# Kernel optimization log

Hardware: AMD Instinct MI355X
Metric: run time of the kernel (lower is better)

## Reference

```python
import jax, jax.numpy as jnp
import numpy as np
import math

H = 12   # num_attention_heads
DH = 64  # attention_head_size
HID = H * DH  # 768


def setup_inputs() -> dict:
    key = jax.random.key(0)
    ks = jax.random.split(key, 16)
    B, S = 2, 128
    inp = {
        'hidden_states': jax.random.normal(ks[0], (B, S, HID), jnp.float32),
        'attention_mask': jnp.zeros((B, 1, 1, S), jnp.float32),
        'inference_path': jax.random.normal(ks[1], (B, S, S, HID), jnp.float32),
        'span_mask': jax.random.uniform(ks[2], (B, 1, S, S), jnp.float32),
    }
    sc = 1.0 / math.sqrt(HID)
    # weights stored as [in, out]; y = x @ W + b
    inp['Wq'] = jax.random.normal(ks[3], (HID, HID), jnp.float32) * sc
    inp['bq'] = jnp.zeros((HID,), jnp.float32)
    inp['Wk'] = jax.random.normal(ks[4], (HID, HID), jnp.float32) * sc
    inp['bk'] = jnp.zeros((HID,), jnp.float32)
    inp['Wv'] = jax.random.normal(ks[5], (HID, HID), jnp.float32) * sc
    inp['bv'] = jnp.zeros((HID,), jnp.float32)
    inp['Wpv'] = jax.random.normal(ks[6], (HID, DH), jnp.float32) * sc
    inp['bpv'] = jnp.zeros((DH,), jnp.float32)
    inp['Wip'] = jax.random.normal(ks[7], (HID, 2 * HID), jnp.float32) * sc
    inp['Wmlp'] = jax.random.normal(ks[8], (HID + DH, HID), jnp.float32) * sc
    inp['bmlp'] = jnp.zeros((HID,), jnp.float32)
    return inp


def reference(hidden_states, attention_mask, inference_path, span_mask,
              Wq, bq, Wk, bk, Wv, bv, Wpv, bpv, Wip, Wmlp, bmlp):
    B, S, _ = hidden_states.shape
    # projections
    q = (hidden_states @ Wq + bq).reshape(B, S, H, DH).transpose(0, 2, 1, 3)  # [B,H,S,Dh]
    k = (hidden_states @ Wk + bk).reshape(B, S, H, DH).transpose(0, 2, 1, 3)
    v = (hidden_states @ Wv + bv).reshape(B, S, H, DH).transpose(0, 2, 1, 3)
    # parse value path: [B,1,S,Dh]
    pv = (hidden_states @ Wpv + bpv).reshape(B, S, 1, DH).transpose(0, 2, 1, 3)
    parse_ctx = jnp.matmul(span_mask, pv)              # [B,1,S,Dh]
    parse_ctx = parse_ctx.transpose(0, 2, 1, 3)        # [B,S,1,Dh]
    # relative inference-path bias: raw view (matches torch .view semantics)
    ip = inference_path @ Wip                           # [B,S,S,2*HID]
    ra, rb = jnp.split(ip, 2, axis=-1)                  # each [B,S,S,HID]
    ra = ra.reshape(B, H, S, S, DH)
    rb = rb.reshape(B, H, S, S, DH)
    qe = q[:, :, :, None, :] + ra                       # [B,H,S,S,Dh]
    ke = k[:, :, None, :, :] + rb                       # [B,H,S,S,Dh]
    scores = jnp.einsum('bhqkd,bhqkd->bhqk', qe, ke)
    scores = scores / math.sqrt(DH) + attention_mask
    probs = jax.nn.softmax(scores, axis=-1)             # dropout is identity in eval
    ctx = jnp.matmul(probs, v)                          # [B,H,S,Dh]
    ctx = ctx.transpose(0, 2, 1, 3)                     # [B,S,H,Dh]
    ctx = jnp.concatenate([ctx, parse_ctx], axis=-2)    # [B,S,H+1,Dh]
    ctx = ctx.reshape(B, S, HID + DH)
    return ctx @ Wmlp + bmlp                            # [B,S,HID]
```

## Files before the change

kernel.cpp:

```cpp
#include <hip/hip_runtime.h>
#include <hip/hip_bf16.h>


typedef __attribute__((ext_vector_type(8))) __bf16 bf16x8;
typedef __attribute__((ext_vector_type(16))) float f32x16;
typedef __attribute__((ext_vector_type(4))) float f32x4;

#define QKV_OFF   0u
#define ARENA_OFF 2424832u
#define SC_OFF    4784128u
#define CTX_OFF   6356992u

__global__ __launch_bounds__(256)
void prep_kernel(const float* __restrict__ Wip, __bf16* __restrict__ arena) {
  const int l = threadIdx.x & 63;
  const int f = blockIdx.x * 4 + (threadIdx.x >> 6);
  const int n32 = f / 48, k16 = f - n32 * 48;
  const float* src = Wip + (size_t)(k16 * 16 + (l >> 5) * 8) * 1536 + n32 * 32 + (l & 31);
  union { __bf16 h[8]; uint4 u; } pk;
#pragma unroll
  for (int j = 0; j < 8; j++) pk.h[j] = (__bf16)src[(size_t)j * 1536];
  ((uint4*)arena)[(size_t)f * 64 + l] = pk.u;
}

__global__ __launch_bounds__(64)
void proj_kernel(const float* __restrict__ hs,
                 const float* __restrict__ Wq, const float* __restrict__ bq,
                 const float* __restrict__ Wk, const float* __restrict__ bk,
                 const float* __restrict__ Wv, const float* __restrict__ bv,
                 const float* __restrict__ Wpv, const float* __restrict__ bpv,
                 float* __restrict__ qkv) {
  const int n0 = blockIdx.x * 32;
  const int m0 = blockIdx.y * 32;
  const float* W; const float* bias; int noff, ldw;
  if (n0 < 768)       { W = Wq;  bias = bq;  noff = n0;        ldw = 768; }
  else if (n0 < 1536) { W = Wk;  bias = bk;  noff = n0 - 768;  ldw = 768; }
  else if (n0 < 2304) { W = Wv;  bias = bv;  noff = n0 - 1536; ldw = 768; }
  else                { W = Wpv; bias = bpv; noff = n0 - 2304; ldw = 64;  }
  const int l = threadIdx.x;
  const int rsel = l & 31, ksel = l >> 5;
  f32x16 acc;
#pragma unroll
  for (int z = 0; z < 16; z++) acc[z] = 0.f;

#pragma unroll 4
  for (int k16 = 0; k16 < 48; k16++) {
    const float* ap = hs + (size_t)(m0 + rsel) * 768 + k16 * 16 + ksel * 8;
    float4 a0 = *(const float4*)ap;
    float4 a1 = *(const float4*)(ap + 4);
    union { __bf16 h[8]; bf16x8 v; } pa;
    pa.h[0] = (__bf16)a0.x; pa.h[1] = (__bf16)a0.y; pa.h[2] = (__bf16)a0.z; pa.h[3] = (__bf16)a0.w;
    pa.h[4] = (__bf16)a1.x; pa.h[5] = (__bf16)a1.y; pa.h[6] = (__bf16)a1.z; pa.h[7] = (__bf16)a1.w;
    const float* bp = W + (size_t)(k16 * 16 + ksel * 8) * ldw + noff + rsel;
    union { __bf16 h[8]; bf16x8 v; } pb;
#pragma unroll
    for (int j = 0; j < 8; j++) pb.h[j] = (__bf16)bp[(size_t)j * ldw];
    acc = __builtin_amdgcn_mfma_f32_32x32x16_bf16(pa.v, pb.v, acc, 0, 0, 0);
  }
#pragma unroll
  for (int reg = 0; reg < 16; reg++) {
    int row = (reg & 3) + ((reg >> 2) << 3) + (ksel << 2);
    qkv[(size_t)(m0 + row) * 2368 + n0 + rsel] = acc[reg] + bias[noff + rsel];
  }
}

extern __shared__ char smem_raw[];

__global__ __launch_bounds__(512, 2)
void score_kernel(const float* __restrict__ infp,
                  const __bf16* __restrict__ arena,
                  const float* __restrict__ qkv,
                  float* __restrict__ scores) {
  char* Abase = smem_raw;
  float* lds_sc = (float*)(smem_raw + 99840);
  const int tid = threadIdx.x;
  const int lane = tid & 63;
  const int ml = lane & 31;
  const int kh = lane >> 5;
  const int wv = tid >> 6;
  const int wc = wv & 3;
  const int wd = wv >> 2;
  const int blk = blockIdx.x;
  const int b = blk >> 8;
  const int r0 = (blk & 255) << 6;

  for (int z = tid; z < 768; z += 512) lds_sc[z] = 0.f;

  const uint4* BA = (const uint4*)arena;
  const uint4* bptr  = BA + (size_t)((2 * wc + wd) * 48) * 64 + lane;
  const uint4* bptr2 = bptr + 73728;
  int kpn = 0;
  uint4 B0[8], B1[8], B2[8];
  bf16x8 Af[8];
  f32x16 acc_ra[2], acc_rb[2];

  auto loadB = [&](uint4* dst) {
#pragma unroll
    for (int ks = 0; ks < 4; ks++) {
      dst[ks * 2]     = bptr[ks * 64];
      dst[ks * 2 + 1] = bptr2[ks * 64];
    }
    if (kpn == 11) { bptr += 21760; bptr2 += 21760; kpn = 0; }
    else           { bptr += 256;   bptr2 += 256;   kpn++;  }
  };

  loadB(B0);
  loadB(B1);

  {
    const f32x4* A4 = (const f32x4*)(infp + (size_t)(b * 16384 + r0) * 768);
#pragma unroll
    for (int p = 0; p < 12; p++) {
      int idx = p * 512 + tid;
      int m = (int)(((unsigned)idx * 10923u) >> 20);
      int g = idx - m * 96;
      f32x4 v0 = __builtin_nontemporal_load(A4 + m * 192 + g * 2);
      f32x4 v1 = __builtin_nontemporal_load(A4 + m * 192 + g * 2 + 1);
      union { __bf16 h[8]; uint4 u; } pk;
      pk.h[0] = (__bf16)v0[0]; pk.h[1] = (__bf16)v0[1];
      pk.h[2] = (__bf16)v0[2]; pk.h[3] = (__bf16)v0[3];
      pk.h[4] = (__bf16)v1[0]; pk.h[5] = (__bf16)v1[1];
      pk.h[6] = (__bf16)v1[2]; pk.h[7] = (__bf16)v1[3];
      int F = (m >> 5) * 48 + (g >> 1);
      int slot = (m & 31) + ((g & 1) << 5);
      *(uint4*)(Abase + ((F * 65 + slot) << 4)) = pk.u;
    }
  }
  __syncthreads();

  const size_t lane_off = (size_t)(lane << 4);
  auto loadA = [&](int kcc) {
    const char* ab = Abase + lane_off + kcc * 4160;
#pragma unroll
    for (int mt = 0; mt < 2; mt++)
#pragma unroll
      for (int ks = 0; ks < 4; ks++)
        Af[mt * 4 + ks] = *(const bf16x8*)(ab + mt * 49920 + ks * 1040);
  };
  auto mfma_step = [&](const uint4* Bb) {
#pragma unroll
    for (int ks = 0; ks < 4; ks++) {
      bf16x8 bra = *(const bf16x8*)&Bb[ks * 2];
      bf16x8 brb = *(const bf16x8*)&Bb[ks * 2 + 1];
#pragma unroll
      for (int mt = 0; mt < 2; mt++) {
        acc_ra[mt] = __builtin_amdgcn_mfma_f32_32x32x16_bf16(Af[mt * 4 + ks], bra, acc_ra[mt], 0, 0, 0);
        acc_rb[mt] = __builtin_amdgcn_mfma_f32_32x32x16_bf16(Af[mt * 4 + ks], brb, acc_rb[mt], 0, 0, 0);
      }
    }
  };
  auto epilogue = [&](int c) {
    int d = wd * 32 + ml;
#pragma unroll
    for (int mt = 0; mt < 2; mt++) {
      float qv[16], kv[16];
#pragma unroll
      for (int reg = 0; reg < 16; reg++) {
        int row = mt * 32 + (reg & 3) + ((reg >> 2) << 3) + (kh << 2);
        int t = 12 * (r0 + row) + c;
        int hh = t >> 14;
        int ii = (t >> 7) & 127;
        int jj = t & 127;
        qv[reg] = qkv[(size_t)((b << 7) + ii) * 2368 + (hh << 6) + d];
        kv[reg] = qkv[(size_t)((b << 7) + jj) * 2368 + 768 + (hh << 6) + d];
      }
#pragma unroll
      for (int reg = 0; reg < 16; reg++) {
        int row = mt * 32 + (reg & 3) + ((reg >> 2) << 3) + (kh << 2);
        float p = (qv[reg] + acc_ra[mt][reg]) * (kv[reg] + acc_rb[mt][reg]);
        p += __shfl_xor(p, 16);
        p += __shfl_xor(p, 8);
        p += __shfl_xor(p, 4);
        p += __shfl_xor(p, 2);
        p += __shfl_xor(p, 1);
        if (ml == 0) atomicAdd(&lds_sc[row * 12 + c], p);
      }
    }
#pragma unroll
    for (int mt = 0; mt < 2; mt++)
#pragma unroll
      for (int z = 0; z < 16; z++) { acc_ra[mt][z] = 0.f; acc_rb[mt][z] = 0.f; }
  };

#pragma unroll
  for (int mt = 0; mt < 2; mt++)
#pragma unroll
    for (int z = 0; z < 16; z++) { acc_ra[mt][z] = 0.f; acc_rb[mt][z] = 0.f; }

  int kcc = 0, cc = wc;
#pragma unroll 1
  for (int it = 0; it < 12; it++) {
    {
      loadB(B2);
      loadA(kcc);
      mfma_step(B0);
      if (kcc == 11) { epilogue(cc); kcc = 0; cc += 4; } else kcc++;
    }
    {
      if (it < 11) loadB(B0);
      loadA(kcc);
      mfma_step(B1);
      if (kcc == 11) { epilogue(cc); kcc = 0; cc += 4; } else kcc++;
    }
    {
      if (it < 11) loadB(B1);
      loadA(kcc);
      mfma_step(B2);
      if (kcc == 11) { epilogue(cc); kcc = 0; cc += 4; } else kcc++;
    }
  }

  __syncthreads();
  for (int z = tid; z < 768; z += 512) {
    int row = z / 12;
    int ccc = z - row * 12;
    int t = 12 * (r0 + row) + ccc;
    int hh = t >> 14;
    int ii = (t >> 7) & 127;
    int jj = t & 127;
    scores[(size_t)((b * 12 + hh) * 128 + ii) * 128 + jj] = lds_sc[z];
  }
}

__global__ __launch_bounds__(256)
void attn_kernel(const float* __restrict__ scores, const float* __restrict__ qkv,
                 const float* __restrict__ mask, const float* __restrict__ span,
                 float* __restrict__ ctx) {
  const int i = blockIdx.x;
  const int b = blockIdx.y;
  const int tid = threadIdx.x;
  const int l = tid & 63;
  const int wvi = tid >> 6;
  __shared__ float w[13][132];
  for (int r = wvi; r < 13; r += 4) {
    if (r < 12) {
      const float* sp = scores + (size_t)((b * 12 + r) * 128 + i) * 128;
      float s0 = sp[l] * 0.125f + mask[b * 128 + l];
      float s1 = sp[l + 64] * 0.125f + mask[b * 128 + l + 64];
      float mx = fmaxf(s0, s1);
#pragma unroll
      for (int o = 32; o; o >>= 1) mx = fmaxf(mx, __shfl_xor(mx, o));
      float e0 = __expf(s0 - mx), e1 = __expf(s1 - mx);
      float sm = e0 + e1;
#pragma unroll
      for (int o = 32; o; o >>= 1) sm += __shfl_xor(sm, o);
      float inv = 1.f / sm;
      w[r][l] = e0 * inv;
      w[r][l + 64] = e1 * inv;
    } else {
      const float* sp = span + (size_t)(b * 128 + i) * 128;
      w[12][l] = sp[l];
      w[12][l + 64] = sp[l + 64];
    }
  }
  __syncthreads();
  for (int o = tid; o < 832; o += 256) {
    int h = o >> 6, d = o & 63;
    const float* vp = qkv + (size_t)(b * 128) * 2368 + (h < 12 ? 1536 + h * 64 : 2304) + d;
    float acc = 0.f;
#pragma unroll 8
    for (int j = 0; j < 128; j++) acc += w[h][j] * vp[(size_t)j * 2368];
    ctx[(size_t)(b * 128 + i) * 832 + o] = acc;
  }
}

__global__ __launch_bounds__(64)
void out_kernel(const float* __restrict__ ctxb, const float* __restrict__ Wmlp,
                const float* __restrict__ bmlp, float* __restrict__ out) {
  const int n0 = blockIdx.x * 32;
  const int m0 = blockIdx.y * 32;
  const int l = threadIdx.x;
  const int rsel = l & 31, ksel = l >> 5;
  f32x16 acc;
#pragma unroll
  for (int z = 0; z < 16; z++) acc[z] = 0.f;

#pragma unroll 4
  for (int k16 = 0; k16 < 52; k16++) {
    const float* ap = ctxb + (size_t)(m0 + rsel) * 832 + k16 * 16 + ksel * 8;
    float4 a0 = *(const float4*)ap;
    float4 a1 = *(const float4*)(ap + 4);
    union { __bf16 h[8]; bf16x8 v; } pa;
    pa.h[0] = (__bf16)a0.x; pa.h[1] = (__bf16)a0.y; pa.h[2] = (__bf16)a0.z; pa.h[3] = (__bf16)a0.w;
    pa.h[4] = (__bf16)a1.x; pa.h[5] = (__bf16)a1.y; pa.h[6] = (__bf16)a1.z; pa.h[7] = (__bf16)a1.w;
    const float* bp = Wmlp + (size_t)(k16 * 16 + ksel * 8) * 768 + n0 + rsel;
    union { __bf16 h[8]; bf16x8 v; } pb;
#pragma unroll
    for (int j = 0; j < 8; j++) pb.h[j] = (__bf16)bp[(size_t)j * 768];
    acc = __builtin_amdgcn_mfma_f32_32x32x16_bf16(pa.v, pb.v, acc, 0, 0, 0);
  }
#pragma unroll
  for (int reg = 0; reg < 16; reg++) {
    int row = (reg & 3) + ((reg >> 2) << 3) + (ksel << 2);
    out[(size_t)(m0 + row) * 768 + n0 + rsel] = acc[reg] + bmlp[n0 + rsel];
  }
}

extern "C" void kernel_launch(void* const* d_in, const int* in_sizes, int n_in,
                              void* d_out, int out_size, void* d_ws, size_t ws_size,
                              hipStream_t stream) {
  const float* hs   = (const float*)d_in[0];
  const float* mask = (const float*)d_in[1];
  const float* infp = (const float*)d_in[2];
  const float* span = (const float*)d_in[3];
  const float* Wq   = (const float*)d_in[4];
  const float* bq   = (const float*)d_in[5];
  const float* Wk   = (const float*)d_in[6];
  const float* bk   = (const float*)d_in[7];
  const float* Wv   = (const float*)d_in[8];
  const float* bv   = (const float*)d_in[9];
  const float* Wpv  = (const float*)d_in[10];
  const float* bpv  = (const float*)d_in[11];
  const float* Wip  = (const float*)d_in[12];
  const float* Wmlp = (const float*)d_in[13];
  const float* bmlp = (const float*)d_in[14];
  float* out = (float*)d_out;

  char* ws = (char*)d_ws;
  float*  qkv    = (float*)(ws + QKV_OFF);
  __bf16* arena  = (__bf16*)(ws + ARENA_OFF);
  float*  scores = (float*)(ws + SC_OFF);
  float*  ctx    = (float*)(ws + CTX_OFF);

  prep_kernel<<<dim3(576), 256, 0, stream>>>(Wip, arena);
  proj_kernel<<<dim3(74, 8), 64, 0, stream>>>(hs, Wq, bq, Wk, bk, Wv, bv, Wpv, bpv, qkv);
  score_kernel<<<dim3(512), 512, 102912, stream>>>(infp, arena, qkv, scores);
  attn_kernel<<<dim3(128, 2), 256, 0, stream>>>(scores, qkv, mask, span, ctx);
  out_kernel<<<dim3(24, 8), 64, 0, stream>>>(ctx, Wmlp, bmlp, out);
}
```

Measured before the change: 354.3 us.

## Merge prep and projection kernels, move P·V to MFMA, widen out blocks

```diff
diff --git a/kernel.cpp b/kernel.cpp
--- a/kernel.cpp
+++ b/kernel.cpp
@@ -12,32 +12,33 @@
 #define CTX_OFF   6356992u
 
 __global__ __launch_bounds__(256)
-void prep_kernel(const float* __restrict__ Wip, __bf16* __restrict__ arena) {
-  const int l = threadIdx.x & 63;
-  const int f = blockIdx.x * 4 + (threadIdx.x >> 6);
-  const int n32 = f / 48, k16 = f - n32 * 48;
-  const float* src = Wip + (size_t)(k16 * 16 + (l >> 5) * 8) * 1536 + n32 * 32 + (l & 31);
-  union { __bf16 h[8]; uint4 u; } pk;
-#pragma unroll
-  for (int j = 0; j < 8; j++) pk.h[j] = (__bf16)src[(size_t)j * 1536];
-  ((uint4*)arena)[(size_t)f * 64 + l] = pk.u;
-}
-
-__global__ __launch_bounds__(64)
-void proj_kernel(const float* __restrict__ hs,
-                 const float* __restrict__ Wq, const float* __restrict__ bq,
-                 const float* __restrict__ Wk, const float* __restrict__ bk,
-                 const float* __restrict__ Wv, const float* __restrict__ bv,
-                 const float* __restrict__ Wpv, const float* __restrict__ bpv,
-                 float* __restrict__ qkv) {
-  const int n0 = blockIdx.x * 32;
-  const int m0 = blockIdx.y * 32;
+void prep_proj_kernel(const float* __restrict__ Wip, __bf16* __restrict__ arena,
+                      const float* __restrict__ hs,
+                      const float* __restrict__ Wq, const float* __restrict__ bq,
+                      const float* __restrict__ Wk, const float* __restrict__ bk,
+                      const float* __restrict__ Wv, const float* __restrict__ bv,
+                      const float* __restrict__ Wpv, const float* __restrict__ bpv,
+                      float* __restrict__ qkv) {
+  if (blockIdx.x < 576) {
+    const int l = threadIdx.x & 63;
+    const int f = blockIdx.x * 4 + (threadIdx.x >> 6);
+    const int n32 = f / 48, k16 = f - n32 * 48;
+    const float* src = Wip + (size_t)(k16 * 16 + (l >> 5) * 8) * 1536 + n32 * 32 + (l & 31);
+    union { __bf16 h[8]; uint4 u; } pk;
+#pragma unroll
+    for (int j = 0; j < 8; j++) pk.h[j] = (__bf16)src[(size_t)j * 1536];
+    ((uint4*)arena)[(size_t)f * 64 + l] = pk.u;
+    return;
+  }
+  const int pblk = blockIdx.x - 576;
+  const int n0 = (pblk % 74) * 32;
+  const int m0 = (pblk / 74) * 128 + (threadIdx.x >> 6) * 32;
   const float* W; const float* bias; int noff, ldw;
   if (n0 < 768)       { W = Wq;  bias = bq;  noff = n0;        ldw = 768; }
   else if (n0 < 1536) { W = Wk;  bias = bk;  noff = n0 - 768;  ldw = 768; }
   else if (n0 < 2304) { W = Wv;  bias = bv;  noff = n0 - 1536; ldw = 768; }
   else                { W = Wpv; bias = bpv; noff = n0 - 2304; ldw = 64;  }
-  const int l = threadIdx.x;
+  const int l = threadIdx.x & 63;
   const int rsel = l & 31, ksel = l >> 5;
   f32x16 acc;
 #pragma unroll
@@ -140,8 +141,8 @@
   auto mfma_step = [&](const uint4* Bb) {
 #pragma unroll
     for (int ks = 0; ks < 4; ks++) {
-      bf16x8 bra = *(const bf16x8*)&Bb[ks * 2];
-      bf16x8 brb = *(const bf16x8*)&Bb[ks * 2 + 1];
+      bf16x8 bra = __builtin_bit_cast(bf16x8, Bb[ks * 2]);
+      bf16x8 brb = __builtin_bit_cast(bf16x8, Bb[ks * 2 + 1]);
 #pragma unroll
       for (int mt = 0; mt < 2; mt++) {
         acc_ra[mt] = __builtin_amdgcn_mfma_f32_32x32x16_bf16(Af[mt * 4 + ks], bra, acc_ra[mt], 0, 0, 0);
@@ -222,54 +223,91 @@
   }
 }
 
-__global__ __launch_bounds__(256)
+__global__ __launch_bounds__(512)
 void attn_kernel(const float* __restrict__ scores, const float* __restrict__ qkv,
                  const float* __restrict__ mask, const float* __restrict__ span,
                  float* __restrict__ ctx) {
-  const int i = blockIdx.x;
-  const int b = blockIdx.y;
+  __shared__ float w4[4][32][132];
+  const int blk = blockIdx.x;
+  const int b = blk >> 2;
+  const int q0 = (blk & 3) << 5;
   const int tid = threadIdx.x;
-  const int l = tid & 63;
-  const int wvi = tid >> 6;
-  __shared__ float w[13][132];
-  for (int r = wvi; r < 13; r += 4) {
-    if (r < 12) {
-      const float* sp = scores + (size_t)((b * 12 + r) * 128 + i) * 128;
-      float s0 = sp[l] * 0.125f + mask[b * 128 + l];
-      float s1 = sp[l + 64] * 0.125f + mask[b * 128 + l + 64];
-      float mx = fmaxf(s0, s1);
-#pragma unroll
-      for (int o = 32; o; o >>= 1) mx = fmaxf(mx, __shfl_xor(mx, o));
-      float e0 = __expf(s0 - mx), e1 = __expf(s1 - mx);
-      float sm = e0 + e1;
-#pragma unroll
-      for (int o = 32; o; o >>= 1) sm += __shfl_xor(sm, o);
-      float inv = 1.f / sm;
-      w[r][l] = e0 * inv;
-      w[r][l + 64] = e1 * inv;
+  const int lane = tid & 63;
+  const int wv = tid >> 6;
+  const int rsel = lane & 31, ksel = lane >> 5;
+
+#pragma unroll 1
+  for (int rnd = 0; rnd < 4; rnd++) {
+    if (rnd < 3) {
+#pragma unroll 1
+      for (int s = 0; s < 16; s++) {
+        int job = s * 8 + wv;
+        int hq = job >> 5;
+        int i  = job & 31;
+        int h  = rnd * 4 + hq;
+        const float* sp = scores + (size_t)((b * 12 + h) * 128 + (q0 + i)) * 128;
+        float s0 = sp[lane] * 0.125f + mask[b * 128 + lane];
+        float s1 = sp[lane + 64] * 0.125f + mask[b * 128 + lane + 64];
+        float mx = fmaxf(s0, s1);
+#pragma unroll
+        for (int o = 32; o; o >>= 1) mx = fmaxf(mx, __shfl_xor(mx, o));
+        float e0 = __expf(s0 - mx), e1 = __expf(s1 - mx);
+        float sm = e0 + e1;
+#pragma unroll
+        for (int o = 32; o; o >>= 1) sm += __shfl_xor(sm, o);
+        float inv = 1.f / sm;
+        w4[hq][i][lane] = e0 * inv;
+        w4[hq][i][lane + 64] = e1 * inv;
+      }
     } else {
-      const float* sp = span + (size_t)(b * 128 + i) * 128;
-      w[12][l] = sp[l];
-      w[12][l + 64] = sp[l + 64];
-    }
-  }
-  __syncthreads();
-  for (int o = tid; o < 832; o += 256) {
-    int h = o >> 6, d = o & 63;
-    const float* vp = qkv + (size_t)(b * 128) * 2368 + (h < 12 ? 1536 + h * 64 : 2304) + d;
-    float acc = 0.f;
-#pragma unroll 8
-    for (int j = 0; j < 128; j++) acc += w[h][j] * vp[(size_t)j * 2368];
-    ctx[(size_t)(b * 128 + i) * 832 + o] = acc;
-  }
-}
-
-__global__ __launch_bounds__(64)
+#pragma unroll 1
+      for (int s = 0; s < 4; s++) {
+        int i = s * 8 + wv;
+        const float* sp = span + (size_t)(b * 16384) + (size_t)(q0 + i) * 128;
+        w4[0][i][lane] = sp[lane];
+        w4[0][i][lane + 64] = sp[lane + 64];
+      }
+    }
+    __syncthreads();
+    const int njobs = (rnd < 3) ? 8 : 2;
+    if (wv < njobs) {
+      const int hq = wv >> 1, nt = wv & 1;
+      int vcol, ocol;
+      if (rnd < 3) { int h = rnd * 4 + hq; vcol = 1536 + h * 64 + nt * 32; ocol = h * 64 + nt * 32; }
+      else         { vcol = 2304 + nt * 32; ocol = 768 + nt * 32; }
+      f32x16 acc;
+#pragma unroll
+      for (int z = 0; z < 16; z++) acc[z] = 0.f;
+#pragma unroll
+      for (int k16 = 0; k16 < 8; k16++) {
+        const float* ap = &w4[hq][rsel][k16 * 16 + ksel * 8];
+        float4 a0 = *(const float4*)ap;
+        float4 a1 = *(const float4*)(ap + 4);
+        union { __bf16 h[8]; bf16x8 v; } pa;
+        pa.h[0] = (__bf16)a0.x; pa.h[1] = (__bf16)a0.y; pa.h[2] = (__bf16)a0.z; pa.h[3] = (__bf16)a0.w;
+        pa.h[4] = (__bf16)a1.x; pa.h[5] = (__bf16)a1.y; pa.h[6] = (__bf16)a1.z; pa.h[7] = (__bf16)a1.w;
+        const float* bp = qkv + (size_t)(b * 128 + k16 * 16 + ksel * 8) * 2368 + vcol + rsel;
+        union { __bf16 h[8]; bf16x8 v; } pb;
+#pragma unroll
+        for (int j = 0; j < 8; j++) pb.h[j] = (__bf16)bp[(size_t)j * 2368];
+        acc = __builtin_amdgcn_mfma_f32_32x32x16_bf16(pa.v, pb.v, acc, 0, 0, 0);
+      }
+#pragma unroll
+      for (int reg = 0; reg < 16; reg++) {
+        int row = (reg & 3) + ((reg >> 2) << 3) + (ksel << 2);
+        ctx[(size_t)(b * 128 + q0 + row) * 832 + ocol + rsel] = acc[reg];
+      }
+    }
+    __syncthreads();
+  }
+}
+
+__global__ __launch_bounds__(256)
 void out_kernel(const float* __restrict__ ctxb, const float* __restrict__ Wmlp,
                 const float* __restrict__ bmlp, float* __restrict__ out) {
   const int n0 = blockIdx.x * 32;
-  const int m0 = blockIdx.y * 32;
-  const int l = threadIdx.x;
+  const int m0 = blockIdx.y * 128 + (threadIdx.x >> 6) * 32;
+  const int l = threadIdx.x & 63;
   const int rsel = l & 31, ksel = l >> 5;
   f32x16 acc;
 #pragma unroll
@@ -322,9 +360,9 @@
   float*  scores = (float*)(ws + SC_OFF);
   float*  ctx    = (float*)(ws + CTX_OFF);
 
-  prep_kernel<<<dim3(576), 256, 0, stream>>>(Wip, arena);
-  proj_kernel<<<dim3(74, 8), 64, 0, stream>>>(hs, Wq, bq, Wk, bk, Wv, bv, Wpv, bpv, qkv);
+  prep_proj_kernel<<<dim3(724), 256, 0, stream>>>(Wip, arena, hs,
+      Wq, bq, Wk, bk, Wv, bv, Wpv, bpv, qkv);
   score_kernel<<<dim3(512), 512, 102912, stream>>>(infp, arena, qkv, scores);
-  attn_kernel<<<dim3(128, 2), 256, 0, stream>>>(scores, qkv, mask, span, ctx);
-  out_kernel<<<dim3(24, 8), 64, 0, stream>>>(ctx, Wmlp, bmlp, out);
-}
+  attn_kernel<<<dim3(8), 512, 0, stream>>>(scores, qkv, mask, span, ctx);
+  out_kernel<<<dim3(24, 2), 256, 0, stream>>>(ctx, Wmlp, bmlp, out);
+}
```

After: 368.2 us. 1.04x slower.
